# Performance work log

Measured on AMD Instinct MI355X. Metric: run time of the kernel, lower is better.

The kernel has to match this reference:

```python
import jax, jax.numpy as jnp
import numpy as np

NUM_HEADS = 12

def setup_inputs() -> dict:
    key = jax.random.key(0)
    k1, k2, k3, k4 = jax.random.split(key, 4)
    B, N, C = 8, 1024, 768
    x = jax.random.normal(k1, (B, N, C), dtype=jnp.float32)
    # torch nn.Linear weights are [out_features, in_features]
    qkv_w = jax.random.normal(k2, (3 * C, C), dtype=jnp.float32) * (1.0 / np.sqrt(C))
    proj_w = jax.random.normal(k3, (C, C), dtype=jnp.float32) * (1.0 / np.sqrt(C))
    proj_b = jax.random.normal(k4, (C,), dtype=jnp.float32) * 0.02
    return {"x": x, "qkv_w": qkv_w, "proj_w": proj_w, "proj_b": proj_b}

def reference(x, qkv_w, proj_w, proj_b):
    B, N, C = x.shape
    H = NUM_HEADS
    D = C // H
    scale = D ** -0.5
    # qkv: [B, N, 3C] -> [3, B, H, N, D]
    qkv = jnp.einsum('bnc,oc->bno', x, qkv_w)
    qkv = qkv.reshape(B, N, 3, H, D).transpose(2, 0, 3, 1, 4)
    q, k, v = qkv[0], qkv[1], qkv[2]
    attn = jnp.einsum('bhnd,bhmd->bhnm', q, k) * scale  # [B,H,N,N]
    attn = jax.nn.softmax(attn, axis=-1)
    # attn_drop is identity at eval (p=0.0)
    out = jnp.einsum('bhnm,bhmd->bhnd', attn, v)  # [B,H,N,D]
    out = out.transpose(0, 2, 1, 3).reshape(B, N, C)
    out = jnp.einsum('bnc,oc->bno', out, proj_w) + proj_b
    # proj_drop is identity at eval (p=0.0)
    return (out, attn)
```

## Files before the change

### kernel.cpp

```cpp
#include <hip/hip_runtime.h>

typedef unsigned short u16;
typedef u16 us8 __attribute__((ext_vector_type(8)));
typedef u16 us4 __attribute__((ext_vector_type(4)));
typedef __bf16 bf16x8 __attribute__((ext_vector_type(8)));
typedef __bf16 bf16x4 __attribute__((ext_vector_type(4)));
typedef float f32x4 __attribute__((ext_vector_type(4)));

static __device__ __forceinline__ u16 f2bf(float f) {
  unsigned int u = __builtin_bit_cast(unsigned int, f);
  u += 0x7fffu + ((u >> 16) & 1u);
  return (u16)(u >> 16);
}

static __device__ __forceinline__ float bf2f(u16 u) {
  return __builtin_bit_cast(float, (unsigned int)u << 16);
}

static __device__ __forceinline__ void gload16(const void* g, void* l) {
  __builtin_amdgcn_global_load_lds((const __attribute__((address_space(1))) void*)g,
                                   (__attribute__((address_space(3))) void*)l,
                                   16, 0, 0);
}

static __device__ __forceinline__ bf16x8 ldfrag_g(const u16* p) {
  return __builtin_bit_cast(bf16x8, *(const us8*)p);
}

template <int N> static __device__ __forceinline__ void vmwait() {
  asm volatile("s_waitcnt vmcnt(%0)" :: "n"(N) : "memory");
}

__global__ void cvt_all(const float* __restrict__ x, const float* __restrict__ wq,
                        const float* __restrict__ wp, u16* __restrict__ xb,
                        u16* __restrict__ wqb, u16* __restrict__ wpb) {
  int i = blockIdx.x * blockDim.x + threadIdx.x;
  const float* s; u16* d; int off;
  if (i < 786432)       { s = x;  d = xb;  off = i; }
  else if (i < 1007616) { s = wq; d = wqb; off = i - 786432; }
  else                  { s = wp; d = wpb; off = i - 1007616; }
  const float4* sp = (const float4*)s + (size_t)off * 2;
  float4 a = sp[0], b = sp[1];
  us8 o;
  o[0] = f2bf(a.x); o[1] = f2bf(a.y); o[2] = f2bf(a.z); o[3] = f2bf(a.w);
  o[4] = f2bf(b.x); o[5] = f2bf(b.y); o[6] = f2bf(b.z); o[7] = f2bf(b.w);
  *((us8*)d + off) = o;
}

template <int MODE>
__global__ __launch_bounds__(256, 4) void gemm_bt(
    const u16* __restrict__ A, const u16* __restrict__ Bt,
    void* __restrict__ Cout, const float* __restrict__ bias,
    u16* __restrict__ vt, int Ncols) {
  __shared__ __align__(16) u16 As[128 * 64];
  __shared__ __align__(16) u16 Bs[128 * 64];
  const int tid = threadIdx.x;
  const int w = tid >> 6, l = tid & 63;
  const int fr = l & 15, fq = l >> 4;
  const int row0 = blockIdx.x * 128;
  const int col0 = blockIdx.y * 128;
  const int wr = (w >> 1) * 64, wc = (w & 1) * 64;
  const int lrow = l >> 3;
  const int lcol = (l & 7) * 8;

  f32x4 acc[4][4];
#pragma unroll
  for (int m = 0; m < 4; ++m)
#pragma unroll
    for (int n = 0; n < 4; ++n) acc[m][n] = f32x4{0.f, 0.f, 0.f, 0.f};

  for (int kt = 0; kt < 12; ++kt) {
    const int k0 = kt * 64;
    __syncthreads();
#pragma unroll
    for (int i = 0; i < 4; ++i) {
      int c = w * 4 + i;
      gload16(A  + (size_t)(row0 + c * 8 + lrow) * 768 + k0 + lcol, &As[c * 512]);
      gload16(Bt + (size_t)(col0 + c * 8 + lrow) * 768 + k0 + lcol, &Bs[c * 512]);
    }
    __syncthreads();
#pragma unroll
    for (int kk = 0; kk < 2; ++kk) {
      bf16x8 a[4], b[4];
#pragma unroll
      for (int m = 0; m < 4; ++m)
        a[m] = __builtin_bit_cast(bf16x8, *(const us8*)&As[(wr + m * 16 + fr) * 64 + kk * 32 + fq * 8]);
#pragma unroll
      for (int n = 0; n < 4; ++n)
        b[n] = __builtin_bit_cast(bf16x8, *(const us8*)&Bs[(wc + n * 16 + fr) * 64 + kk * 32 + fq * 8]);
#pragma unroll
      for (int m = 0; m < 4; ++m)
#pragma unroll
        for (int n = 0; n < 4; ++n)
          acc[m][n] = __builtin_amdgcn_mfma_f32_16x16x32_bf16(a[m], b[n], acc[m][n], 0, 0, 0);
    }
  }

  if (MODE == 0) {
#pragma unroll
    for (int m = 0; m < 4; ++m) {
      int r = row0 + wr + m * 16 + fq * 4;
#pragma unroll
      for (int n = 0; n < 4; ++n) {
        int c = col0 + wc + n * 16 + fr;
        float bb = bias[c];
#pragma unroll
        for (int j = 0; j < 4; ++j)
          ((float*)Cout)[(size_t)(r + j) * Ncols + c] = acc[m][n][j] + bb;
      }
    }
  } else if (col0 < 1536) {
#pragma unroll
    for (int m = 0; m < 4; ++m) {
      int r = row0 + wr + m * 16 + fq * 4;
#pragma unroll
      for (int n = 0; n < 4; ++n) {
        int c = col0 + wc + n * 16 + fr;
#pragma unroll
        for (int j = 0; j < 4; ++j)
          ((u16*)Cout)[(size_t)(r + j) * Ncols + c] = f2bf(acc[m][n][j]);
      }
    }
  } else {
    const int b = row0 >> 10;
#pragma unroll
    for (int m = 0; m < 4; ++m) {
      int r = row0 + wr + m * 16 + fq * 4;
      int n0 = r & 1023;
#pragma unroll
      for (int n = 0; n < 4; ++n) {
        int c = col0 + wc + n * 16 + fr;
        f32x4 v = acc[m][n];
        us4 o2;
        o2[0] = f2bf(v[0]); o2[1] = f2bf(v[1]); o2[2] = f2bf(v[2]); o2[3] = f2bf(v[3]);
        *(us4*)&vt[(size_t)(b * 768 + (c - 1536)) * 1024 + n0] = o2;
      }
    }
  }
}

__global__ __launch_bounds__(256, 2) void attn_fused(
    const u16* __restrict__ qkv, const u16* __restrict__ vt,
    float* __restrict__ attn_out, u16* __restrict__ ctx) {
  __shared__ __align__(16) u16 P[32 * 1024];
  __shared__ float red[2][4][32];
  const int tid = threadIdx.x;
  const int w = tid >> 6, l = tid & 63;
  const int fr = l & 15, fq = l >> 4;
  const int bh = blockIdx.x >> 5;
  const int qt = blockIdx.x & 31;
  const int b = bh / 12, h = bh - b * 12;
  const int q0 = qt * 32;

  bf16x8 aq[2][2];
#pragma unroll
  for (int m = 0; m < 2; ++m)
#pragma unroll
    for (int kk = 0; kk < 2; ++kk)
      aq[m][kk] = ldfrag_g(&qkv[(size_t)(b * 1024 + q0 + m * 16 + fr) * 2304 + h * 64 + kk * 32 + fq * 8]);
  vmwait<0>();
  __builtin_amdgcn_sched_barrier(0);

  char* kbase = (char*)P + w * 16384;
  const int kl = l >> 3;
  const int csrc = ((l & 7) ^ (kl & 7)) * 8;
  const u16* kb = &qkv[(size_t)b * 1024 * 2304 + 768 + h * 64];
  const u16* ksrc = kb + (size_t)(w * 256 + kl) * 2304 + csrc;

  f32x4 acc[16][2];
#pragma unroll
  for (int n = 0; n < 16; ++n)
#pragma unroll
    for (int m = 0; m < 2; ++m) acc[n][m] = f32x4{0.f, 0.f, 0.f, 0.f};

#pragma unroll
  for (int i = 0; i < 8; ++i)
    gload16(ksrc + (size_t)(i * 8) * 2304, kbase + i * 1024);

#pragma unroll
  for (int g = 0; g < 4; ++g) {
    if (g < 3) {
#pragma unroll
      for (int i = 0; i < 8; ++i)
        gload16(ksrc + (size_t)((g + 1) * 64 + i * 8) * 2304,
                kbase + ((g + 1) & 1) * 8192 + i * 1024);
      vmwait<8>();
    } else {
      vmwait<0>();
    }
    __builtin_amdgcn_sched_barrier(0);
    char* buf = kbase + (g & 1) * 8192;
    __builtin_amdgcn_s_setprio(1);
#pragma unroll
    for (int n2 = 0; n2 < 4; ++n2) {
      int rowb = (n2 * 16 + fr) * 128;
#pragma unroll
      for (int kk = 0; kk < 2; ++kk) {
        int cidx = (kk * 4 + fq) ^ (fr & 7);
        bf16x8 bk = __builtin_bit_cast(bf16x8, *(const us8*)(buf + rowb + cidx * 16));
        int n = g * 4 + n2;
        acc[n][0] = __builtin_amdgcn_mfma_f32_16x16x32_bf16(bk, aq[0][kk], acc[n][0], 0, 0, 0);
        acc[n][1] = __builtin_amdgcn_mfma_f32_16x16x32_bf16(bk, aq[1][kk], acc[n][1], 0, 0, 0);
      }
    }
    __builtin_amdgcn_s_setprio(0);
  }

  float mx[2];
#pragma unroll
  for (int m = 0; m < 2; ++m) mx[m] = -3.4e38f;
#pragma unroll
  for (int n = 0; n < 16; ++n)
#pragma unroll
    for (int m = 0; m < 2; ++m) {
      f32x4 v = acc[n][m];
      mx[m] = fmaxf(mx[m], fmaxf(fmaxf(v[0], v[1]), fmaxf(v[2], v[3])));
    }
#pragma unroll
  for (int m = 0; m < 2; ++m) {
    float v = mx[m];
    v = fmaxf(v, __shfl_xor(v, 16));
    v = fmaxf(v, __shfl_xor(v, 32));
    mx[m] = v;
  }
  if (fq == 0) {
#pragma unroll
    for (int m = 0; m < 2; ++m) red[0][w][m * 16 + fr] = mx[m];
  }
  __syncthreads();
  const float C = 0.125f * 1.44269504f;
  float nrm[2];
#pragma unroll
  for (int m = 0; m < 2; ++m) {
    int r = m * 16 + fr;
    float rm = fmaxf(fmaxf(red[0][0][r], red[0][1][r]), fmaxf(red[0][2][r], red[0][3][r]));
    nrm[m] = -rm * C;
  }

  float sum[2] = {0.f, 0.f};
#pragma unroll
  for (int n = 0; n < 16; ++n)
#pragma unroll
    for (int m = 0; m < 2; ++m) {
#pragma unroll
      for (int j = 0; j < 4; ++j) {
        float p = exp2f(fmaf(acc[n][m][j], C, nrm[m]));
        acc[n][m][j] = p;
        sum[m] += p;
      }
    }
#pragma unroll
  for (int m = 0; m < 2; ++m) {
    float v = sum[m];
    v += __shfl_xor(v, 16);
    v += __shfl_xor(v, 32);
    sum[m] = v;
  }
  if (fq == 0) {
#pragma unroll
    for (int m = 0; m < 2; ++m) red[1][w][m * 16 + fr] = sum[m];
  }
  __syncthreads();
  float rinv[2];
#pragma unroll
  for (int m = 0; m < 2; ++m) {
    int r = m * 16 + fr;
    rinv[m] = 1.0f / (red[1][0][r] + red[1][1][r] + red[1][2][r] + red[1][3][r]);
  }

#pragma unroll
  for (int n = 0; n < 16; ++n)
#pragma unroll
    for (int m = 0; m < 2; ++m) {
      int row = m * 16 + fr;
      int key = n * 16 + fq * 4;
      f32x4 v = acc[n][m];
      bf16x4 pk;
      pk[0] = (__bf16)(v[0] * rinv[m]); pk[1] = (__bf16)(v[1] * rinv[m]);
      pk[2] = (__bf16)(v[2] * rinv[m]); pk[3] = (__bf16)(v[3] * rinv[m]);
      int byte = (row * 2048 + (w * 256 + key) * 2) ^ ((row & 7) << 4);
      *(us4*)((char*)P + byte) = __builtin_bit_cast(us4, pk);
    }
  __syncthreads();

  float* aout = attn_out + (size_t)bh * (1024 * 1024) + (size_t)q0 * 1024;
#pragma unroll
  for (int it = 0; it < 32; ++it) {
    int idx = it * 256 + tid;
    int row = idx >> 8;
    int ch = idx & 255;
    int byte = (row * 2048 + ch * 8) ^ ((row & 7) << 4);
    us4 p4 = *(const us4*)((const char*)P + byte);
    f32x4 o;
    o[0] = bf2f(p4[0]); o[1] = bf2f(p4[1]); o[2] = bf2f(p4[2]); o[3] = bf2f(p4[3]);
    __builtin_nontemporal_store(o, (f32x4*)(aout + (size_t)row * 1024 + ch * 4));
  }

  f32x4 o2[2];
  o2[0] = f32x4{0.f, 0.f, 0.f, 0.f};
  o2[1] = f32x4{0.f, 0.f, 0.f, 0.f};
  const u16* vb = &vt[(size_t)bh * 64 * 1024 + (size_t)(w * 16 + fr) * 1024];
#pragma unroll 8
  for (int ks = 0; ks < 32; ++ks) {
    bf16x8 bv = ldfrag_g(&vb[ks * 32 + fq * 8]);
#pragma unroll
    for (int m = 0; m < 2; ++m) {
      int row = m * 16 + fr;
      int byte = (row * 2048 + (ks * 32 + fq * 8) * 2) ^ ((row & 7) << 4);
      bf16x8 ap = __builtin_bit_cast(bf16x8, *(const us8*)((const char*)P + byte));
      o2[m] = __builtin_amdgcn_mfma_f32_16x16x32_bf16(ap, bv, o2[m], 0, 0, 0);
    }
  }
#pragma unroll
  for (int m = 0; m < 2; ++m)
#pragma unroll
    for (int j = 0; j < 4; ++j) {
      int row = q0 + m * 16 + fq * 4 + j;
      int col = h * 64 + w * 16 + fr;
      ctx[(size_t)(b * 1024 + row) * 768 + col] = f2bf(o2[m][j]);
    }
}

extern "C" void kernel_launch(void* const* d_in, const int* in_sizes, int n_in,
                              void* d_out, int out_size, void* d_ws, size_t ws_size,
                              hipStream_t stream) {
  const float* x      = (const float*)d_in[0];
  const float* qkv_w  = (const float*)d_in[1];
  const float* proj_w = (const float*)d_in[2];
  const float* proj_b = (const float*)d_in[3];
  float* out = (float*)d_out;
  float* attn_out = out + 6291456;

  char* ws = (char*)d_ws;
  u16* qkv_bf = (u16*)(ws);
  u16* x_bf   = (u16*)(ws + 37748736);
  u16* wq_bf  = (u16*)(ws + 50331648);
  u16* wp_bf  = (u16*)(ws + 53870592);
  u16* vt_bf  = (u16*)(ws + 55050240);
  u16* ctx_bf = (u16*)(ws + 67633152);

  cvt_all<<<4224, 256, 0, stream>>>(x, qkv_w, proj_w, x_bf, wq_bf, wp_bf);

  gemm_bt<1><<<dim3(64, 18), 256, 0, stream>>>(x_bf, wq_bf, qkv_bf, nullptr, vt_bf, 2304);
  attn_fused<<<3072, 256, 0, stream>>>(qkv_bf, vt_bf, attn_out, ctx_bf);
  gemm_bt<0><<<dim3(64, 6), 256, 0, stream>>>(ctx_bf, wp_bf, out, proj_b, nullptr, 768);
}
```

Measured before the change: 190.3 us.

## Use single-wave 64x64 GEMM blocks with double-buffered async LDS loads

Both GEMMs switch from 256-thread, 128x128 tiles to one-wavefront blocks computing 64x64 tiles. The LDS buffers are double-buffered, and the loads for the next k-tile are issued before computing the current one, waiting through vmcnt instead of using block barriers. This is meant to remove __syncthreads stalls and overlap global-to-LDS transfers with MFMA work, and it launches four times as many blocks. In exchange, each block reuses its A and B tiles over fewer outputs, so more is read from L2 overall. The correctness of the vmwait counts depends on the single-wave ordering.

```diff
diff --git a/kernel.cpp b/kernel.cpp
--- a/kernel.cpp
+++ b/kernel.cpp
@@ -48,46 +48,57 @@
 }
 
 template <int MODE>
-__global__ __launch_bounds__(256, 4) void gemm_bt(
+__global__ __launch_bounds__(64) void gemm_1w(
     const u16* __restrict__ A, const u16* __restrict__ Bt,
     void* __restrict__ Cout, const float* __restrict__ bias,
     u16* __restrict__ vt, int Ncols) {
-  __shared__ __align__(16) u16 As[128 * 64];
-  __shared__ __align__(16) u16 Bs[128 * 64];
-  const int tid = threadIdx.x;
-  const int w = tid >> 6, l = tid & 63;
+  __shared__ __align__(16) u16 As[2][64 * 64];
+  __shared__ __align__(16) u16 Bs[2][64 * 64];
+  const int l = threadIdx.x;
   const int fr = l & 15, fq = l >> 4;
-  const int row0 = blockIdx.x * 128;
-  const int col0 = blockIdx.y * 128;
-  const int wr = (w >> 1) * 64, wc = (w & 1) * 64;
+  const int row0 = blockIdx.x * 64;
+  const int col0 = blockIdx.y * 64;
   const int lrow = l >> 3;
   const int lcol = (l & 7) * 8;
 
+  const u16* Ab = A  + (size_t)(row0 + lrow) * 768 + lcol;
+  const u16* Bb = Bt + (size_t)(col0 + lrow) * 768 + lcol;
+
   f32x4 acc[4][4];
 #pragma unroll
   for (int m = 0; m < 4; ++m)
 #pragma unroll
     for (int n = 0; n < 4; ++n) acc[m][n] = f32x4{0.f, 0.f, 0.f, 0.f};
 
+#pragma unroll
+  for (int i = 0; i < 8; ++i) {
+    gload16(Ab + (size_t)(i * 8) * 768, &As[0][i * 512]);
+    gload16(Bb + (size_t)(i * 8) * 768, &Bs[0][i * 512]);
+  }
+
   for (int kt = 0; kt < 12; ++kt) {
-    const int k0 = kt * 64;
-    __syncthreads();
-#pragma unroll
-    for (int i = 0; i < 4; ++i) {
-      int c = w * 4 + i;
-      gload16(A  + (size_t)(row0 + c * 8 + lrow) * 768 + k0 + lcol, &As[c * 512]);
-      gload16(Bt + (size_t)(col0 + c * 8 + lrow) * 768 + k0 + lcol, &Bs[c * 512]);
-    }
-    __syncthreads();
+    const int cur = kt & 1;
+    if (kt < 11) {
+      const int k1 = (kt + 1) * 64;
+#pragma unroll
+      for (int i = 0; i < 8; ++i) {
+        gload16(Ab + (size_t)(i * 8) * 768 + k1, &As[cur ^ 1][i * 512]);
+        gload16(Bb + (size_t)(i * 8) * 768 + k1, &Bs[cur ^ 1][i * 512]);
+      }
+      vmwait<16>();
+    } else {
+      vmwait<0>();
+    }
+    __builtin_amdgcn_sched_barrier(0);
 #pragma unroll
     for (int kk = 0; kk < 2; ++kk) {
       bf16x8 a[4], b[4];
 #pragma unroll
       for (int m = 0; m < 4; ++m)
-        a[m] = __builtin_bit_cast(bf16x8, *(const us8*)&As[(wr + m * 16 + fr) * 64 + kk * 32 + fq * 8]);
+        a[m] = __builtin_bit_cast(bf16x8, *(const us8*)&As[cur][(m * 16 + fr) * 64 + kk * 32 + fq * 8]);
 #pragma unroll
       for (int n = 0; n < 4; ++n)
-        b[n] = __builtin_bit_cast(bf16x8, *(const us8*)&Bs[(wc + n * 16 + fr) * 64 + kk * 32 + fq * 8]);
+        b[n] = __builtin_bit_cast(bf16x8, *(const us8*)&Bs[cur][(n * 16 + fr) * 64 + kk * 32 + fq * 8]);
 #pragma unroll
       for (int m = 0; m < 4; ++m)
 #pragma unroll
@@ -99,10 +110,10 @@
   if (MODE == 0) {
 #pragma unroll
     for (int m = 0; m < 4; ++m) {
-      int r = row0 + wr + m * 16 + fq * 4;
+      int r = row0 + m * 16 + fq * 4;
 #pragma unroll
       for (int n = 0; n < 4; ++n) {
-        int c = col0 + wc + n * 16 + fr;
+        int c = col0 + n * 16 + fr;
         float bb = bias[c];
 #pragma unroll
         for (int j = 0; j < 4; ++j)
@@ -112,10 +123,10 @@
   } else if (col0 < 1536) {
 #pragma unroll
     for (int m = 0; m < 4; ++m) {
-      int r = row0 + wr + m * 16 + fq * 4;
+      int r = row0 + m * 16 + fq * 4;
 #pragma unroll
       for (int n = 0; n < 4; ++n) {
-        int c = col0 + wc + n * 16 + fr;
+        int c = col0 + n * 16 + fr;
 #pragma unroll
         for (int j = 0; j < 4; ++j)
           ((u16*)Cout)[(size_t)(r + j) * Ncols + c] = f2bf(acc[m][n][j]);
@@ -125,11 +136,11 @@
     const int b = row0 >> 10;
 #pragma unroll
     for (int m = 0; m < 4; ++m) {
-      int r = row0 + wr + m * 16 + fq * 4;
+      int r = row0 + m * 16 + fq * 4;
       int n0 = r & 1023;
 #pragma unroll
       for (int n = 0; n < 4; ++n) {
-        int c = col0 + wc + n * 16 + fr;
+        int c = col0 + n * 16 + fr;
         f32x4 v = acc[m][n];
         us4 o2;
         o2[0] = f2bf(v[0]); o2[1] = f2bf(v[1]); o2[2] = f2bf(v[2]); o2[3] = f2bf(v[3]);
@@ -291,9 +302,9 @@
     int ch = idx & 255;
     int byte = (row * 2048 + ch * 8) ^ ((row & 7) << 4);
     us4 p4 = *(const us4*)((const char*)P + byte);
-    f32x4 o;
-    o[0] = bf2f(p4[0]); o[1] = bf2f(p4[1]); o[2] = bf2f(p4[2]); o[3] = bf2f(p4[3]);
-    __builtin_nontemporal_store(o, (f32x4*)(aout + (size_t)row * 1024 + ch * 4));
+    f32x4 o2;
+    o2[0] = bf2f(p4[0]); o2[1] = bf2f(p4[1]); o2[2] = bf2f(p4[2]); o2[3] = bf2f(p4[3]);
+    __builtin_nontemporal_store(o2, (f32x4*)(aout + (size_t)row * 1024 + ch * 4));
   }
 
   f32x4 o2[2];
@@ -341,7 +352,7 @@
 
   cvt_all<<<4224, 256, 0, stream>>>(x, qkv_w, proj_w, x_bf, wq_bf, wp_bf);
 
-  gemm_bt<1><<<dim3(64, 18), 256, 0, stream>>>(x_bf, wq_bf, qkv_bf, nullptr, vt_bf, 2304);
+  gemm_1w<1><<<dim3(128, 36), 64, 0, stream>>>(x_bf, wq_bf, qkv_bf, nullptr, vt_bf, 2304);
   attn_fused<<<3072, 256, 0, stream>>>(qkv_bf, vt_bf, attn_out, ctx_bf);
-  gemm_bt<0><<<dim3(64, 6), 256, 0, stream>>>(ctx_bf, wp_bf, out, proj_b, nullptr, 768);
-}
+  gemm_1w<0><<<dim3(128, 12), 64, 0, stream>>>(ctx_bf, wp_bf, out, proj_b, nullptr, 768);
+}
```

New measurement: 217.3 us. 14.2% more time.
